# Performance work log

Hardware: AMD Instinct MI355X
Metric: run time of the kernel (lower is better)

The kernel has to match this reference:

```python
import jax, jax.numpy as jnp
import numpy as np

N_ATOMS = 8_000_000
N_REC = 2_000_000
N_POC = 500_000
N_CHAINS = 4


def setup_inputs() -> dict:
    key = jax.random.key(0)
    k1, k2, k3, k4 = jax.random.split(key, 4)
    # coordinates in nm, inside a ~5 nm box
    positions = jax.random.uniform(k1, (N_ATOMS, 3), dtype=jnp.float32) * 5.0
    box_vectors = jnp.diag(jnp.array([5.0, 5.0, 5.0], dtype=jnp.float32))
    # unique receptor atom indices into positions
    rec_indices = jax.random.permutation(k2, N_ATOMS)[:N_REC].astype(jnp.int32)
    # unique pocket indices INTO THE REC ARRAY (poc_pos = rec_pos[poc_indices])
    poc_indices = jax.random.permutation(k3, N_REC)[:N_POC].astype(jnp.int32)
    # contiguous chain assignment over rec atoms, all chains present in pocket
    chain_ids = ((jnp.arange(N_REC, dtype=jnp.int32) * N_CHAINS) // N_REC).astype(jnp.int32)
    poc_chain_ids = chain_ids[poc_indices]
    ref_poc = jax.random.uniform(k4, (N_POC, 3), dtype=jnp.float32) * 5.0
    k = jnp.float32(100.0)  # kJ/mol/nm^2
    return {
        "positions": positions, "box_vectors": box_vectors, "ref_poc": ref_poc,
        "k": k, "rec_indices": rec_indices, "poc_indices": poc_indices,
        "chain_ids": chain_ids, "poc_chain_ids": poc_chain_ids, "n_chains": N_CHAINS,
    }


def best_periodic_translation(pos1, pos2, box_vectors):
    # pos1, pos2: [C,3]; box_vectors: [3,3] (rows are lattice vectors)
    delta = pos2 - pos1
    inv = 1.0 / jnp.diag(box_vectors)
    s3 = jnp.round(delta[:, 2] * inv[2])
    delta = delta - s3[:, None] * box_vectors[2]
    s2 = jnp.round(delta[:, 1] * inv[1])
    delta = delta - s2[:, None] * box_vectors[1]
    s1 = jnp.round(delta[:, 0] * inv[0])
    return s1[:, None] * box_vectors[0] + s2[:, None] * box_vectors[1] + s3[:, None] * box_vectors[2]


def reference(positions, box_vectors, ref_poc, k, rec_indices, poc_indices, chain_ids, poc_chain_ids, n_chains):
    rec_pos = positions[rec_indices]  # [R,3]
    # Per-chain pocket COM. NOTE: original indexes global positions here
    # (positions[poc_chain_indices]), NOT rec_pos -- reproduced faithfully.
    poc_glob = positions[poc_indices]  # [P,3]
    counts = jax.ops.segment_sum(jnp.ones((poc_glob.shape[0],), poc_glob.dtype), poc_chain_ids, num_segments=n_chains)  # [C]
    poc_com = jax.ops.segment_sum(poc_glob, poc_chain_ids, num_segments=n_chains) / counts[:, None]  # [C,3]
    ref_com = jax.ops.segment_sum(ref_poc, poc_chain_ids, num_segments=n_chains) / counts[:, None]  # [C,3]
    best_t = best_periodic_translation(poc_com, ref_com, box_vectors)  # [C,3]
    rec_pos = rec_pos + best_t[chain_ids]  # translate each chain into the reference image

    poc_pos = rec_pos[poc_indices]  # [P,3]
    rec_origin = jnp.mean(rec_pos, axis=0)
    rec_centered = rec_pos - rec_origin
    r_sq = jnp.sum(rec_centered ** 2, axis=1)  # [R]
    F = jnp.zeros_like(rec_pos).at[poc_indices].set(-2.0 * k * (poc_pos - ref_poc))
    F_mean = jnp.mean(F, axis=0)
    torque = jnp.cross(rec_centered, F)
    torque_mean = jnp.mean(torque, axis=0)
    F_rot = jnp.cross(torque_mean[None], rec_centered) / r_sq[:, None]
    F_final = jnp.zeros_like(positions).at[rec_indices].set(F_mean + F_rot)
    return (jnp.float32(0.0), F_final)
```

## Files before the change

kernel.cpp:

```cpp
#include <hip/hip_runtime.h>


typedef unsigned int uint32;
typedef unsigned char uchar;

#define MAXC 16
#define W_BT 0
#define W_O 48
#define W_FM 52
#define W_TM 56
#define W_ACC 64

#define GCOUNT_OFF 4096
#define REC_OFF 8192
#define NB 512
#define BSH 14
#define BUCKET_ATOMS (1 << BSH)
#define CAP 5120
#define INV8_OFF (REC_OFF + NB * CAP * 4)

#define PB 512
#define RB 512
#define K1_KPT 16
#define K1_CHUNK (256 * K1_KPT)

struct PartSh { uint32 hist[NB]; uint32 curs[NB]; uint32 base[NB]; };
struct PocSh  { float red[4][43]; float accL[3 + MAXC * 10]; };
union ShU { PartSh part; PocSh poc; };

__device__ inline float waveSum(float v) {
#pragma unroll
  for (int off = 32; off > 0; off >>= 1) v += __shfl_down(v, off, 64);
  return v;
}

__global__ __launch_bounds__(256) void k_fused(
    const float* __restrict__ pos, const float* __restrict__ ref_poc,
    const int* __restrict__ rec_idx, const int* __restrict__ cid,
    const int* __restrict__ poc_idx, const int* __restrict__ poc_cid,
    const int* __restrict__ ncp, int R, int P,
    uint32* __restrict__ gcount, uint32* __restrict__ grecords,
    float* __restrict__ ws) {
  const int tid = threadIdx.x;
  const int bid = blockIdx.x;
  __shared__ ShU sh;
  const int C = ncp[0];

  if (bid < PB) {
    const int gsz = PB * 256;
    if (C <= 4) {
      float vals[43];
#pragma unroll
      for (int v = 0; v < 43; ++v) vals[v] = 0.f;
      for (int rb = bid * 256 + tid; rb < P; rb += 4 * gsz) {
        int rr[4], i2[4], c2[4], ri[4];
        float g[4][3], p[4][3], rf[4][3];
#pragma unroll
        for (int q = 0; q < 4; ++q) {
          int r = rb + q * gsz;
          rr[q] = (r < P) ? r : -1;
        }
#pragma unroll
        for (int q = 0; q < 4; ++q) {
          int r = (rr[q] < 0) ? 0 : rr[q];
          i2[q] = poc_idx[r];
          c2[q] = poc_cid[r];
        }
#pragma unroll
        for (int q = 0; q < 4; ++q) {
          ri[q] = rec_idx[i2[q]];
          g[q][0] = pos[3 * i2[q] + 0];
          g[q][1] = pos[3 * i2[q] + 1];
          g[q][2] = pos[3 * i2[q] + 2];
        }
#pragma unroll
        for (int q = 0; q < 4; ++q) {
          int r = (rr[q] < 0) ? 0 : rr[q];
          p[q][0] = pos[3 * ri[q] + 0];
          p[q][1] = pos[3 * ri[q] + 1];
          p[q][2] = pos[3 * ri[q] + 2];
          rf[q][0] = ref_poc[3 * r + 0];
          rf[q][1] = ref_poc[3 * r + 1];
          rf[q][2] = ref_poc[3 * r + 2];
        }
#pragma unroll
        for (int q = 0; q < 4; ++q) {
          if (rr[q] >= 0) {
            vals[0] += p[q][1] * rf[q][2] - p[q][2] * rf[q][1];
            vals[1] += p[q][2] * rf[q][0] - p[q][0] * rf[q][2];
            vals[2] += p[q][0] * rf[q][1] - p[q][1] * rf[q][0];
#pragma unroll
            for (int cc = 0; cc < 4; ++cc) {
              bool m = (c2[q] == cc);
              float* a = &vals[3 + cc * 10];
              a[0] += m ? g[q][0] : 0.f; a[1] += m ? g[q][1] : 0.f;
              a[2] += m ? g[q][2] : 0.f;
              a[3] += m ? rf[q][0] : 0.f; a[4] += m ? rf[q][1] : 0.f;
              a[5] += m ? rf[q][2] : 0.f;
              a[6] += m ? p[q][0] : 0.f; a[7] += m ? p[q][1] : 0.f;
              a[8] += m ? p[q][2] : 0.f;
              a[9] += m ? 1.f : 0.f;
            }
          }
        }
      }
      const int wid = tid >> 6;
#pragma unroll
      for (int v = 0; v < 43; ++v) {
        float s = waveSum(vals[v]);
        if ((tid & 63) == 0) sh.poc.red[wid][v] = s;
      }
      __syncthreads();
      for (int t = tid; t < 43; t += 256)
        atomicAdd(&ws[W_ACC + 19 + t], sh.poc.red[0][t] + sh.poc.red[1][t] +
                                       sh.poc.red[2][t] + sh.poc.red[3][t]);
    } else {
      float* accL = sh.poc.accL;
      for (int t = tid; t < 3 + MAXC * 10; t += 256) accL[t] = 0.f;
      __syncthreads();
      for (int r = bid * 256 + tid; r < P; r += PB * 256) {
        int i2 = poc_idx[r];
        int c2 = poc_cid[r];
        int ri = rec_idx[i2];
        float gx = pos[3 * i2 + 0], gy = pos[3 * i2 + 1], gz = pos[3 * i2 + 2];
        float px = pos[3 * ri + 0], py = pos[3 * ri + 1], pz = pos[3 * ri + 2];
        float rx = ref_poc[3 * r + 0], ry = ref_poc[3 * r + 1], rz = ref_poc[3 * r + 2];
        atomicAdd(&accL[0], py * rz - pz * ry);
        atomicAdd(&accL[1], pz * rx - px * rz);
        atomicAdd(&accL[2], px * ry - py * rx);
        float* a = &accL[3 + c2 * 10];
        atomicAdd(&a[0], gx); atomicAdd(&a[1], gy); atomicAdd(&a[2], gz);
        atomicAdd(&a[3], rx); atomicAdd(&a[4], ry); atomicAdd(&a[5], rz);
        atomicAdd(&a[6], px); atomicAdd(&a[7], py); atomicAdd(&a[8], pz);
        atomicAdd(&a[9], 1.f);
      }
      __syncthreads();
      for (int t = tid; t < 3 + MAXC * 10; t += 256)
        if (accL[t] != 0.f) atomicAdd(&ws[W_ACC + 19 + t], accL[t]);
    }
  } else {
    const int pb = bid - PB;
    uint32* hist = sh.part.hist;
    uint32* curs = sh.part.curs;
    uint32* base = sh.part.base;
    for (int r0 = pb * K1_CHUNK; r0 < R; r0 += RB * K1_CHUNK) {
      int cnt = R - r0; if (cnt > K1_CHUNK) cnt = K1_CHUNK;
      for (int t = tid; t < NB; t += 256) { hist[t] = 0u; curs[t] = 0u; }
      __syncthreads();
      uint32 enc[K1_KPT];
#pragma unroll
      for (int j = 0; j < K1_KPT; ++j) {
        int t = tid + j * 256;
        uint32 e = 0xFFFFFFFFu;
        if (t < cnt) {
          uint32 idx = (uint32)rec_idx[r0 + t];
          uint32 c = (uint32)cid[r0 + t] & 255u;
          e = (idx << 8) | c;
          atomicAdd(&hist[idx >> BSH], 1u);
        }
        enc[j] = e;
      }
      __syncthreads();
      for (int t = tid; t < NB; t += 256) {
        uint32 h = hist[t];
        base[t] = h ? atomicAdd(&gcount[t], h) : 0u;
      }
      __syncthreads();
#pragma unroll
      for (int j = 0; j < K1_KPT; ++j) {
        uint32 e = enc[j];
        if (e != 0xFFFFFFFFu) {
          uint32 b = e >> (8 + BSH);
          uint32 slot = base[b] + atomicAdd(&curs[b], 1u);
          if (slot < CAP) grecords[b * CAP + slot] = e;
        }
      }
      __syncthreads();
    }
  }
}

__global__ __launch_bounds__(256) void k_bucket_build(
    const float4* __restrict__ pos4, const int* __restrict__ ncp,
    const uint32* __restrict__ gcount, const uint32* __restrict__ grecords,
    int N, uchar* __restrict__ inv8, float* __restrict__ ws) {
  const int tid = threadIdx.x;
  const int b = blockIdx.x;
  const int a0 = b << BSH;
  if (a0 >= N) return;
  int natoms = N - a0; if (natoms > BUCKET_ATOMS) natoms = BUCKET_ATOMS;

  __shared__ uchar map_[BUCKET_ATOMS];
  __shared__ float cnt16[MAXC];
  uint4* m16 = (uint4*)map_;
  uint4 ff; ff.x = ff.y = ff.z = ff.w = 0xFFFFFFFFu;
  for (int t = tid; t < BUCKET_ATOMS / 16; t += 256) m16[t] = ff;
  const int C = ncp[0];
  if (C > 4) for (int t = tid; t < MAXC; t += 256) cnt16[t] = 0.f;
  __syncthreads();

  int n = (int)gcount[b]; if (n > CAP) n = CAP;
  float c0 = 0.f, c1 = 0.f, c2 = 0.f, c3 = 0.f;
  for (int t = tid; t < n; t += 256) {
    uint32 e = grecords[b * CAP + t];
    uint32 ia = (e >> 8) & (BUCKET_ATOMS - 1);
    uint32 c = e & 255u;
    map_[ia] = (uchar)c;
    if (C <= 4) {
      c0 += (c == 0u) ? 1.f : 0.f;
      c1 += (c == 1u) ? 1.f : 0.f;
      c2 += (c == 2u) ? 1.f : 0.f;
      c3 += (c == 3u) ? 1.f : 0.f;
    } else {
      atomicAdd(&cnt16[c], 1.f);
    }
  }
  __syncthreads();

  uchar* dst = inv8 + a0;
  if (natoms == BUCKET_ATOMS) {
    uint4* d16 = (uint4*)dst;
    for (int t = tid; t < BUCKET_ATOMS / 16; t += 256) d16[t] = m16[t];
  } else {
    for (int t = tid; t < natoms; t += 256) dst[t] = map_[t];
  }

  float sx = 0.f, sy = 0.f, sz = 0.f;
  int ngf = natoms >> 2;
  const uchar4* m4 = (const uchar4*)map_;
  int g0 = a0 >> 2;
  for (int g = tid; g < ngf; g += 256) {
    float4 p0 = pos4[3 * (g0 + g) + 0];
    float4 p1 = pos4[3 * (g0 + g) + 1];
    float4 p2 = pos4[3 * (g0 + g) + 2];
    uchar4 m = m4[g];
    if (m.x != 255) { sx += p0.x; sy += p0.y; sz += p0.z; }
    if (m.y != 255) { sx += p0.w; sy += p1.x; sz += p1.y; }
    if (m.z != 255) { sx += p1.z; sy += p1.w; sz += p2.x; }
    if (m.w != 255) { sx += p2.y; sy += p2.z; sz += p2.w; }
  }
  int tb = natoms & 3;
  if (tid < tb) {
    int a = a0 + (ngf << 2) + tid;
    const float* pf = (const float*)pos4;
    if (map_[(ngf << 2) + tid] != 255) {
      sx += pf[3 * a]; sy += pf[3 * a + 1]; sz += pf[3 * a + 2];
    }
  }

  __shared__ float red[4][7];
  float vv[7] = {sx, sy, sz, c0, c1, c2, c3};
  const int wid = tid >> 6;
#pragma unroll
  for (int v = 0; v < 7; ++v) {
    float s = waveSum(vv[v]);
    if ((tid & 63) == 0) red[wid][v] = s;
  }
  __syncthreads();
  if (tid < 7) {
    float s = red[0][tid] + red[1][tid] + red[2][tid] + red[3][tid];
    atomicAdd(&ws[W_ACC + tid], s);
  }
  if (C > 4 && tid < C) atomicAdd(&ws[W_ACC + 3 + tid], cnt16[tid]);
}

__global__ void k_finalize(const float* __restrict__ box,
                           const float* __restrict__ kp,
                           const int* __restrict__ ncp,
                           int R, float* __restrict__ ws) {
  __shared__ float tot[192];
  const int C = ncp[0];
  for (int t = threadIdx.x; t < 192; t += blockDim.x) tot[t] = ws[W_ACC + t];
  __syncthreads();
  if (threadIdx.x != 0) return;
  const float kk = kp[0];
  const float Rf = (float)R;
  const float* xp = &tot[19];
  float inv0 = 1.f / box[0], inv1 = 1.f / box[4], inv2 = 1.f / box[8];
  float ox = tot[0], oy = tot[1], oz = tot[2];
  float Fx = 0, Fy = 0, Fz = 0;
  float T1x = 0, T1y = 0, T1z = 0, T2x = 0, T2y = 0, T2z = 0;
  for (int c = 0; c < C; ++c) {
    float nrec = tot[3 + c];
    const float* a = &tot[22 + c * 10];
    float np = a[9];
    float invn = 1.f / np;
    float pcx = a[0] * invn, pcy = a[1] * invn, pcz = a[2] * invn;
    float rcx = a[3] * invn, rcy = a[4] * invn, rcz = a[5] * invn;
    float dx = rcx - pcx, dy = rcy - pcy, dz = rcz - pcz;
    float s3 = rintf(dz * inv2);
    dx -= s3 * box[6]; dy -= s3 * box[7]; dz -= s3 * box[8];
    float s2 = rintf(dy * inv1);
    dx -= s2 * box[3]; dy -= s2 * box[4]; dz -= s2 * box[5];
    float s1 = rintf(dx * inv0);
    float btx = s1 * box[0] + s2 * box[3] + s3 * box[6];
    float bty = s1 * box[1] + s2 * box[4] + s3 * box[7];
    float btz = s1 * box[2] + s2 * box[5] + s3 * box[8];
    ws[W_BT + c * 3 + 0] = btx;
    ws[W_BT + c * 3 + 1] = bty;
    ws[W_BT + c * 3 + 2] = btz;
    ox += nrec * btx; oy += nrec * bty; oz += nrec * btz;
    float SFx = -2.f * kk * (a[6] + np * btx - a[3]);
    float SFy = -2.f * kk * (a[7] + np * bty - a[4]);
    float SFz = -2.f * kk * (a[8] + np * btz - a[5]);
    Fx += SFx; Fy += SFy; Fz += SFz;
    T1x += a[7] * btz - a[8] * bty;
    T1y += a[8] * btx - a[6] * btz;
    T1z += a[6] * bty - a[7] * btx;
    T2x += bty * SFz - btz * SFy;
    T2y += btz * SFx - btx * SFz;
    T2z += btx * SFy - bty * SFx;
  }
  ox /= Rf; oy /= Rf; oz /= Rf;
  float Tx = 2.f * kk * xp[0] - 2.f * kk * T1x + T2x - (oy * Fz - oz * Fy);
  float Ty = 2.f * kk * xp[1] - 2.f * kk * T1y + T2y - (oz * Fx - ox * Fz);
  float Tz = 2.f * kk * xp[2] - 2.f * kk * T1z + T2z - (ox * Fy - oy * Fx);
  ws[W_O + 0] = ox; ws[W_O + 1] = oy; ws[W_O + 2] = oz;
  ws[W_FM + 0] = Fx / Rf; ws[W_FM + 1] = Fy / Rf; ws[W_FM + 2] = Fz / Rf;
  ws[W_TM + 0] = Tx / Rf; ws[W_TM + 1] = Ty / Rf; ws[W_TM + 2] = Tz / Rf;
}

__global__ __launch_bounds__(256) void k_final_dense(
    const float* __restrict__ pos, const uchar* __restrict__ inv8,
    int N, const float* __restrict__ ws, float* __restrict__ out) {
  __shared__ float stage[3328];
  __shared__ float sc[64];
  const int tid = threadIdx.x;
  if (tid < 64) sc[tid] = ws[tid];
  const int t0 = blockIdx.x * 1024;
  int nat = N - t0; if (nat > 1024) nat = 1024;
  const int nfl = nat * 3;

  if (nat == 1024) {
    const float4* src4 = (const float4*)(pos + 3 * t0);
#pragma unroll
    for (int kk = 0; kk < 3; ++kk) {
      int v4 = tid + kk * 256;
      float4 p = src4[v4];
      int idx = 4 * v4 + v4 / 3;
      stage[idx + 0] = p.x; stage[idx + 1] = p.y;
      stage[idx + 2] = p.z; stage[idx + 3] = p.w;
    }
  } else {
    for (int k = tid; k < nfl; k += 256)
      stage[k + (int)((unsigned)k / 12u)] = pos[3 * t0 + k];
  }
  __syncthreads();

  float ox = sc[W_O + 0], oy = sc[W_O + 1], oz = sc[W_O + 2];
  float fmx = sc[W_FM + 0], fmy = sc[W_FM + 1], fmz = sc[W_FM + 2];
  float tmx = sc[W_TM + 0], tmy = sc[W_TM + 1], tmz = sc[W_TM + 2];

  uchar mc[4];
  if (nat == 1024) {
    uchar4 m = ((const uchar4*)(inv8 + t0))[tid];
    mc[0] = m.x; mc[1] = m.y; mc[2] = m.z; mc[3] = m.w;
  } else {
#pragma unroll
    for (int q = 0; q < 4; ++q) {
      int la = 4 * tid + q;
      mc[q] = (la < nat) ? inv8[t0 + la] : (uchar)255;
    }
  }
#pragma unroll
  for (int q = 0; q < 4; ++q) {
    int la = 4 * tid + q;
    if (la < nat) {
      float* s = &stage[13 * tid + 3 * q];
      float fx = 0.f, fy = 0.f, fz = 0.f;
      int c = mc[q];
      if (c != 255) {
        float cx = s[0] + sc[W_BT + 3 * c + 0] - ox;
        float cy = s[1] + sc[W_BT + 3 * c + 1] - oy;
        float cz = s[2] + sc[W_BT + 3 * c + 2] - oz;
        float inv = 1.f / (cx * cx + cy * cy + cz * cz);
        fx = fmx + (tmy * cz - tmz * cy) * inv;
        fy = fmy + (tmz * cx - tmx * cz) * inv;
        fz = fmz + (tmx * cy - tmy * cx) * inv;
      }
      s[0] = fx; s[1] = fy; s[2] = fz;
    }
  }
  __syncthreads();

  if (blockIdx.x == 0 && tid == 0) out[0] = 0.f;
  float* ob = out + 1 + 3 * t0;
  if (nat == 1024) {
#pragma unroll
    for (int kk = 0; kk < 3; ++kk) {
      int j = tid + kk * 256;
      if (j < 767) {
        int k = 3 + 4 * j;
        float4 v;
        v.x = stage[k + k / 12];
        v.y = stage[(k + 1) + (k + 1) / 12];
        v.z = stage[(k + 2) + (k + 2) / 12];
        v.w = stage[(k + 3) + (k + 3) / 12];
        *(float4*)(ob + k) = v;
      }
    }
    if (tid < 3) ob[tid] = stage[tid];
    if (tid == 3) ob[3071] = stage[3071 + 3071 / 12];
  } else {
    for (int k = tid; k < nfl; k += 256)
      ob[k] = stage[k + (int)((unsigned)k / 12u)];
  }
}

extern "C" void kernel_launch(void* const* d_in, const int* in_sizes, int n_in,
                              void* d_out, int out_size, void* d_ws, size_t ws_size,
                              hipStream_t stream) {
  const float* pos     = (const float*)d_in[0];
  const float* box     = (const float*)d_in[1];
  const float* ref_poc = (const float*)d_in[2];
  const float* kp      = (const float*)d_in[3];
  const int* rec_idx   = (const int*)d_in[4];
  const int* poc_idx   = (const int*)d_in[5];
  const int* cid       = (const int*)d_in[6];
  const int* poc_cid   = (const int*)d_in[7];
  const int* ncp       = (const int*)d_in[8];
  float* out = (float*)d_out;
  float* ws  = (float*)d_ws;
  uint32* gcount   = (uint32*)((char*)d_ws + GCOUNT_OFF);
  uint32* grecords = (uint32*)((char*)d_ws + REC_OFF);
  uchar* inv8      = (uchar*)d_ws + INV8_OFF;

  const int N = in_sizes[0] / 3;
  const int R = in_sizes[4];
  const int P = in_sizes[5];

  hipMemsetAsync(d_ws, 0, 8192, stream);

  k_fused<<<PB + RB, 256, 0, stream>>>(pos, ref_poc, rec_idx, cid, poc_idx,
                                       poc_cid, ncp, R, P, gcount, grecords, ws);
  k_bucket_build<<<NB, 256, 0, stream>>>((const float4*)pos, ncp, gcount,
                                         grecords, N, inv8, ws);
  k_finalize<<<1, 256, 0, stream>>>(box, kp, ncp, R, ws);
  int gF = (N + 1023) / 1024;
  k_final_dense<<<gF, 256, 0, stream>>>(pos, inv8, N, ws, out);
}
```

Baseline: 267.4 us.

## Fuse all phases into one persistent kernel with software grid barriers

Merges the partition, bucket-build, finalize and dense output kernels into a single persistent kernel sized from occupancy. The phases are separated by atomic spin grid barriers, which removes three kernel launch gaps and the tail drain between them. It also halves the bucket size (1024 buckets of 8192 atoms), moves the per-chain receptor counts into the partition phase, and splits blocks 5:3 between pocket and partition work. The risks are spin-barrier overhead, a possible deadlock if not every block is co-resident, and lower parallelism in the later phases because the grid is capped at 1024 blocks.

Result: slower. 287.7 us (+7.6%).

```diff
diff --git a/kernel.cpp b/kernel.cpp
--- a/kernel.cpp
+++ b/kernel.cpp
@@ -11,22 +11,24 @@
 #define W_TM 56
 #define W_ACC 64
 
+#define BAR_OFF 4032
 #define GCOUNT_OFF 4096
 #define REC_OFF 8192
-#define NB 512
-#define BSH 14
+#define NBK 1024
+#define BSH 13
 #define BUCKET_ATOMS (1 << BSH)
-#define CAP 5120
-#define INV8_OFF (REC_OFF + NB * CAP * 4)
-
-#define PB 512
-#define RB 512
+#define CAP 2560
+#define INV8_OFF (REC_OFF + NBK * CAP * 4)
+
 #define K1_KPT 16
 #define K1_CHUNK (256 * K1_KPT)
 
-struct PartSh { uint32 hist[NB]; uint32 curs[NB]; uint32 base[NB]; };
+struct PartSh { uint32 hist[NBK]; uint32 curs[NBK]; uint32 base[NBK]; };
 struct PocSh  { float red[4][43]; float accL[3 + MAXC * 10]; };
-union ShU { PartSh part; PocSh poc; };
+struct MapSh  { uchar map_[BUCKET_ATOMS]; };
+struct StageSh{ float stage[3328]; };
+union ShU { PartSh part; PocSh poc; MapSh map; StageSh st; };
+struct MiscSh { float red7[4][7]; float sc[64]; float cnt16[MAXC]; float tot[192]; };
 
 __device__ inline float waveSum(float v) {
 #pragma unroll
@@ -34,20 +36,36 @@
   return v;
 }
 
-__global__ __launch_bounds__(256) void k_fused(
-    const float* __restrict__ pos, const float* __restrict__ ref_poc,
-    const int* __restrict__ rec_idx, const int* __restrict__ cid,
-    const int* __restrict__ poc_idx, const int* __restrict__ poc_cid,
-    const int* __restrict__ ncp, int R, int P,
-    uint32* __restrict__ gcount, uint32* __restrict__ grecords,
-    float* __restrict__ ws) {
+__device__ inline void gridBar(uint32* bar, int nblk, uint32 phase) {
+  __threadfence();
+  __syncthreads();
+  if (threadIdx.x == 0) {
+    __hip_atomic_fetch_add(bar, 1u, __ATOMIC_ACQ_REL, __HIP_MEMORY_SCOPE_AGENT);
+    const uint32 tgt = (uint32)nblk * phase;
+    for (int it = 0; it < (1 << 21); ++it) {
+      if (__hip_atomic_load(bar, __ATOMIC_ACQUIRE, __HIP_MEMORY_SCOPE_AGENT) >= tgt)
+        break;
+      __builtin_amdgcn_s_sleep(8);
+    }
+  }
+  __syncthreads();
+  __threadfence();
+}
+
+__device__ void phaseA(const float* __restrict__ pos,
+                       const float* __restrict__ ref_poc,
+                       const int* __restrict__ rec_idx,
+                       const int* __restrict__ cid,
+                       const int* __restrict__ poc_idx,
+                       const int* __restrict__ poc_cid,
+                       int C, int R, int P,
+                       uint32* __restrict__ gcount,
+                       uint32* __restrict__ grecords,
+                       float* __restrict__ ws,
+                       ShU& sh, MiscSh& ms, int bid, int pbN, int rbN) {
   const int tid = threadIdx.x;
-  const int bid = blockIdx.x;
-  __shared__ ShU sh;
-  const int C = ncp[0];
-
-  if (bid < PB) {
-    const int gsz = PB * 256;
+  if (bid < pbN) {
+    const int gsz = pbN * 256;
     if (C <= 4) {
       float vals[43];
 #pragma unroll
@@ -118,7 +136,7 @@
       float* accL = sh.poc.accL;
       for (int t = tid; t < 3 + MAXC * 10; t += 256) accL[t] = 0.f;
       __syncthreads();
-      for (int r = bid * 256 + tid; r < P; r += PB * 256) {
+      for (int r = bid * 256 + tid; r < P; r += pbN * 256) {
         int i2 = poc_idx[r];
         int c2 = poc_cid[r];
         int ri = rec_idx[i2];
@@ -139,13 +157,18 @@
         if (accL[t] != 0.f) atomicAdd(&ws[W_ACC + 19 + t], accL[t]);
     }
   } else {
-    const int pb = bid - PB;
+    const int pb = bid - pbN;
     uint32* hist = sh.part.hist;
     uint32* curs = sh.part.curs;
     uint32* base = sh.part.base;
-    for (int r0 = pb * K1_CHUNK; r0 < R; r0 += RB * K1_CHUNK) {
+    float c0 = 0.f, c1 = 0.f, c2 = 0.f, c3 = 0.f;
+    if (C > 4) {
+      for (int t = tid; t < MAXC; t += 256) ms.cnt16[t] = 0.f;
+      __syncthreads();
+    }
+    for (int r0 = pb * K1_CHUNK; r0 < R; r0 += rbN * K1_CHUNK) {
       int cnt = R - r0; if (cnt > K1_CHUNK) cnt = K1_CHUNK;
-      for (int t = tid; t < NB; t += 256) { hist[t] = 0u; curs[t] = 0u; }
+      for (int t = tid; t < NBK; t += 256) { hist[t] = 0u; curs[t] = 0u; }
       __syncthreads();
       uint32 enc[K1_KPT];
 #pragma unroll
@@ -157,11 +180,17 @@
           uint32 c = (uint32)cid[r0 + t] & 255u;
           e = (idx << 8) | c;
           atomicAdd(&hist[idx >> BSH], 1u);
+          if (C <= 4) {
+            c0 += (c == 0u) ? 1.f : 0.f; c1 += (c == 1u) ? 1.f : 0.f;
+            c2 += (c == 2u) ? 1.f : 0.f; c3 += (c == 3u) ? 1.f : 0.f;
+          } else {
+            atomicAdd(&ms.cnt16[c], 1.f);
+          }
         }
         enc[j] = e;
       }
       __syncthreads();
-      for (int t = tid; t < NB; t += 256) {
+      for (int t = tid; t < NBK; t += 256) {
         uint32 h = hist[t];
         base[t] = h ? atomicAdd(&gcount[t], h) : 0u;
       }
@@ -177,102 +206,102 @@
       }
       __syncthreads();
     }
-  }
-}
-
-__global__ __launch_bounds__(256) void k_bucket_build(
-    const float4* __restrict__ pos4, const int* __restrict__ ncp,
-    const uint32* __restrict__ gcount, const uint32* __restrict__ grecords,
-    int N, uchar* __restrict__ inv8, float* __restrict__ ws) {
+    if (C <= 4) {
+      float vv[4] = {c0, c1, c2, c3};
+      const int wid = tid >> 6;
+#pragma unroll
+      for (int v = 0; v < 4; ++v) {
+        float s = waveSum(vv[v]);
+        if ((tid & 63) == 0) ms.red7[wid][v] = s;
+      }
+      __syncthreads();
+      if (tid < 4)
+        atomicAdd(&ws[W_ACC + 3 + tid], ms.red7[0][tid] + ms.red7[1][tid] +
+                                        ms.red7[2][tid] + ms.red7[3][tid]);
+    } else {
+      __syncthreads();
+      if (tid < C) atomicAdd(&ws[W_ACC + 3 + tid], ms.cnt16[tid]);
+    }
+  }
+}
+
+__device__ void phaseBC(const float* __restrict__ pos,
+                        const uint32* __restrict__ gcount,
+                        const uint32* __restrict__ grecords,
+                        int N, uchar* __restrict__ inv8,
+                        float* __restrict__ ws,
+                        ShU& sh, MiscSh& ms, int bid, int gridN) {
   const int tid = threadIdx.x;
-  const int b = blockIdx.x;
-  const int a0 = b << BSH;
-  if (a0 >= N) return;
-  int natoms = N - a0; if (natoms > BUCKET_ATOMS) natoms = BUCKET_ATOMS;
-
-  __shared__ uchar map_[BUCKET_ATOMS];
-  __shared__ float cnt16[MAXC];
-  uint4* m16 = (uint4*)map_;
-  uint4 ff; ff.x = ff.y = ff.z = ff.w = 0xFFFFFFFFu;
-  for (int t = tid; t < BUCKET_ATOMS / 16; t += 256) m16[t] = ff;
-  const int C = ncp[0];
-  if (C > 4) for (int t = tid; t < MAXC; t += 256) cnt16[t] = 0.f;
+  float sx = 0.f, sy = 0.f, sz = 0.f;
+  for (int b = bid; b < NBK; b += gridN) {
+    const int a0 = b << BSH;
+    if (a0 >= N) break;
+    int natoms = N - a0; if (natoms > BUCKET_ATOMS) natoms = BUCKET_ATOMS;
+    uchar* map_ = sh.map.map_;
+    uint4* m16 = (uint4*)map_;
+    uint4 ff; ff.x = ff.y = ff.z = ff.w = 0xFFFFFFFFu;
+    for (int t = tid; t < BUCKET_ATOMS / 16; t += 256) m16[t] = ff;
+    __syncthreads();
+    int n = (int)gcount[b]; if (n > CAP) n = CAP;
+    for (int t = tid; t < n; t += 256) {
+      uint32 e = grecords[b * CAP + t];
+      map_[(e >> 8) & (BUCKET_ATOMS - 1)] = (uchar)(e & 255u);
+    }
+    __syncthreads();
+    uchar* dst = inv8 + a0;
+    if (natoms == BUCKET_ATOMS) {
+      uint4* d16 = (uint4*)dst;
+      for (int t = tid; t < BUCKET_ATOMS / 16; t += 256) d16[t] = m16[t];
+    } else {
+      for (int t = tid; t < natoms; t += 256) dst[t] = map_[t];
+    }
+    int ngf = natoms >> 2;
+    const uchar4* m4 = (const uchar4*)map_;
+    const float4* pos4 = (const float4*)pos;
+    int g0 = a0 >> 2;
+    for (int g = tid; g < ngf; g += 256) {
+      float4 p0 = pos4[3 * (g0 + g) + 0];
+      float4 p1 = pos4[3 * (g0 + g) + 1];
+      float4 p2 = pos4[3 * (g0 + g) + 2];
+      uchar4 m = m4[g];
+      if (m.x != 255) { sx += p0.x; sy += p0.y; sz += p0.z; }
+      if (m.y != 255) { sx += p0.w; sy += p1.x; sz += p1.y; }
+      if (m.z != 255) { sx += p1.z; sy += p1.w; sz += p2.x; }
+      if (m.w != 255) { sx += p2.y; sy += p2.z; sz += p2.w; }
+    }
+    int tb = natoms & 3;
+    if (tid < tb) {
+      int a = a0 + (ngf << 2) + tid;
+      if (map_[(ngf << 2) + tid] != 255) {
+        sx += pos[3 * a]; sy += pos[3 * a + 1]; sz += pos[3 * a + 2];
+      }
+    }
+    __syncthreads();
+  }
+  float vv[3] = {sx, sy, sz};
+  const int wid = tid >> 6;
+#pragma unroll
+  for (int v = 0; v < 3; ++v) {
+    float s = waveSum(vv[v]);
+    if ((tid & 63) == 0) ms.red7[wid][v] = s;
+  }
   __syncthreads();
-
-  int n = (int)gcount[b]; if (n > CAP) n = CAP;
-  float c0 = 0.f, c1 = 0.f, c2 = 0.f, c3 = 0.f;
-  for (int t = tid; t < n; t += 256) {
-    uint32 e = grecords[b * CAP + t];
-    uint32 ia = (e >> 8) & (BUCKET_ATOMS - 1);
-    uint32 c = e & 255u;
-    map_[ia] = (uchar)c;
-    if (C <= 4) {
-      c0 += (c == 0u) ? 1.f : 0.f;
-      c1 += (c == 1u) ? 1.f : 0.f;
-      c2 += (c == 2u) ? 1.f : 0.f;
-      c3 += (c == 3u) ? 1.f : 0.f;
-    } else {
-      atomicAdd(&cnt16[c], 1.f);
-    }
-  }
+  if (tid < 3) {
+    float s = ms.red7[0][tid] + ms.red7[1][tid] + ms.red7[2][tid] + ms.red7[3][tid];
+    if (s != 0.f) atomicAdd(&ws[W_ACC + tid], s);
+  }
+}
+
+__device__ void phaseFZ(const float* __restrict__ box,
+                        const float* __restrict__ kp,
+                        int C, int R, float* __restrict__ ws,
+                        MiscSh& ms, int bid) {
+  if (bid != 0) return;
+  const int tid = threadIdx.x;
+  for (int t = tid; t < 192; t += 256) ms.tot[t] = ws[W_ACC + t];
   __syncthreads();
-
-  uchar* dst = inv8 + a0;
-  if (natoms == BUCKET_ATOMS) {
-    uint4* d16 = (uint4*)dst;
-    for (int t = tid; t < BUCKET_ATOMS / 16; t += 256) d16[t] = m16[t];
-  } else {
-    for (int t = tid; t < natoms; t += 256) dst[t] = map_[t];
-  }
-
-  float sx = 0.f, sy = 0.f, sz = 0.f;
-  int ngf = natoms >> 2;
-  const uchar4* m4 = (const uchar4*)map_;
-  int g0 = a0 >> 2;
-  for (int g = tid; g < ngf; g += 256) {
-    float4 p0 = pos4[3 * (g0 + g) + 0];
-    float4 p1 = pos4[3 * (g0 + g) + 1];
-    float4 p2 = pos4[3 * (g0 + g) + 2];
-    uchar4 m = m4[g];
-    if (m.x != 255) { sx += p0.x; sy += p0.y; sz += p0.z; }
-    if (m.y != 255) { sx += p0.w; sy += p1.x; sz += p1.y; }
-    if (m.z != 255) { sx += p1.z; sy += p1.w; sz += p2.x; }
-    if (m.w != 255) { sx += p2.y; sy += p2.z; sz += p2.w; }
-  }
-  int tb = natoms & 3;
-  if (tid < tb) {
-    int a = a0 + (ngf << 2) + tid;
-    const float* pf = (const float*)pos4;
-    if (map_[(ngf << 2) + tid] != 255) {
-      sx += pf[3 * a]; sy += pf[3 * a + 1]; sz += pf[3 * a + 2];
-    }
-  }
-
-  __shared__ float red[4][7];
-  float vv[7] = {sx, sy, sz, c0, c1, c2, c3};
-  const int wid = tid >> 6;
-#pragma unroll
-  for (int v = 0; v < 7; ++v) {
-    float s = waveSum(vv[v]);
-    if ((tid & 63) == 0) red[wid][v] = s;
-  }
-  __syncthreads();
-  if (tid < 7) {
-    float s = red[0][tid] + red[1][tid] + red[2][tid] + red[3][tid];
-    atomicAdd(&ws[W_ACC + tid], s);
-  }
-  if (C > 4 && tid < C) atomicAdd(&ws[W_ACC + 3 + tid], cnt16[tid]);
-}
-
-__global__ void k_finalize(const float* __restrict__ box,
-                           const float* __restrict__ kp,
-                           const int* __restrict__ ncp,
-                           int R, float* __restrict__ ws) {
-  __shared__ float tot[192];
-  const int C = ncp[0];
-  for (int t = threadIdx.x; t < 192; t += blockDim.x) tot[t] = ws[W_ACC + t];
-  __syncthreads();
-  if (threadIdx.x != 0) return;
+  if (tid != 0) return;
+  float* tot = ms.tot;
   const float kk = kp[0];
   const float Rf = (float)R;
   const float* xp = &tot[19];
@@ -320,91 +349,162 @@
   ws[W_TM + 0] = Tx / Rf; ws[W_TM + 1] = Ty / Rf; ws[W_TM + 2] = Tz / Rf;
 }
 
-__global__ __launch_bounds__(256) void k_final_dense(
+__device__ void phaseD(const float* __restrict__ pos,
+                       const uchar* __restrict__ inv8,
+                       int N, const float* __restrict__ ws,
+                       float* __restrict__ out,
+                       ShU& sh, MiscSh& ms, int bid, int gridN) {
+  const int tid = threadIdx.x;
+  float* sc = ms.sc;
+  if (tid < 64) sc[tid] = ws[tid];
+  if (bid == 0 && tid == 0) out[0] = 0.f;
+  const int ntiles = (N + 1023) >> 10;
+  for (int tile = bid; tile < ntiles; tile += gridN) {
+    const int t0 = tile << 10;
+    int nat = N - t0; if (nat > 1024) nat = 1024;
+    const int nfl = nat * 3;
+    float* stage = sh.st.stage;
+
+    if (nat == 1024) {
+      const float4* src4 = (const float4*)(pos + 3 * t0);
+#pragma unroll
+      for (int kk = 0; kk < 3; ++kk) {
+        int v4 = tid + kk * 256;
+        float4 p = src4[v4];
+        int idx = 4 * v4 + v4 / 3;
+        stage[idx + 0] = p.x; stage[idx + 1] = p.y;
+        stage[idx + 2] = p.z; stage[idx + 3] = p.w;
+      }
+    } else {
+      for (int k = tid; k < nfl; k += 256)
+        stage[k + (int)((unsigned)k / 12u)] = pos[3 * t0 + k];
+    }
+    __syncthreads();
+
+    float ox = sc[W_O + 0], oy = sc[W_O + 1], oz = sc[W_O + 2];
+    float fmx = sc[W_FM + 0], fmy = sc[W_FM + 1], fmz = sc[W_FM + 2];
+    float tmx = sc[W_TM + 0], tmy = sc[W_TM + 1], tmz = sc[W_TM + 2];
+
+    uchar mc[4];
+    if (nat == 1024) {
+      uchar4 m = ((const uchar4*)(inv8 + t0))[tid];
+      mc[0] = m.x; mc[1] = m.y; mc[2] = m.z; mc[3] = m.w;
+    } else {
+#pragma unroll
+      for (int q = 0; q < 4; ++q) {
+        int la = 4 * tid + q;
+        mc[q] = (la < nat) ? inv8[t0 + la] : (uchar)255;
+      }
+    }
+#pragma unroll
+    for (int q = 0; q < 4; ++q) {
+      int la = 4 * tid + q;
+      if (la < nat) {
+        float* s = &stage[13 * tid + 3 * q];
+        float fx = 0.f, fy = 0.f, fz = 0.f;
+        int c = mc[q];
+        if (c != 255) {
+          float cx = s[0] + sc[W_BT + 3 * c + 0] - ox;
+          float cy = s[1] + sc[W_BT + 3 * c + 1] - oy;
+          float cz = s[2] + sc[W_BT + 3 * c + 2] - oz;
+          float inv = 1.f / (cx * cx + cy * cy + cz * cz);
+          fx = fmx + (tmy * cz - tmz * cy) * inv;
+          fy = fmy + (tmz * cx - tmx * cz) * inv;
+          fz = fmz + (tmx * cy - tmy * cx) * inv;
+        }
+        s[0] = fx; s[1] = fy; s[2] = fz;
+      }
+    }
+    __syncthreads();
+
+    float* ob = out + 1 + 3 * t0;
+    if (nat == 1024) {
+#pragma unroll
+      for (int kk = 0; kk < 3; ++kk) {
+        int j = tid + kk * 256;
+        if (j < 767) {
+          int k = 3 + 4 * j;
+          float4 v;
+          v.x = stage[k + k / 12];
+          v.y = stage[(k + 1) + (k + 1) / 12];
+          v.z = stage[(k + 2) + (k + 2) / 12];
+          v.w = stage[(k + 3) + (k + 3) / 12];
+          *(float4*)(ob + k) = v;
+        }
+      }
+      if (tid < 3) ob[tid] = stage[tid];
+      if (tid == 3) ob[3071] = stage[3071 + 3071 / 12];
+    } else {
+      for (int k = tid; k < nfl; k += 256)
+        ob[k] = stage[k + (int)((unsigned)k / 12u)];
+    }
+    __syncthreads();
+  }
+}
+
+__global__ __launch_bounds__(256, 4) void k_all(
+    const float* __restrict__ pos, const float* __restrict__ ref_poc,
+    const int* __restrict__ rec_idx, const int* __restrict__ cid,
+    const int* __restrict__ poc_idx, const int* __restrict__ poc_cid,
+    const int* __restrict__ ncp, const float* __restrict__ box,
+    const float* __restrict__ kp, int R, int P, int N,
+    uint32* __restrict__ gcount, uint32* __restrict__ grecords,
+    uchar* __restrict__ inv8, float* __restrict__ ws,
+    float* __restrict__ out, uint32* __restrict__ bar) {
+  __shared__ ShU sh;
+  __shared__ MiscSh ms;
+  const int bid = blockIdx.x;
+  const int gridN = gridDim.x;
+  const int pbN = (gridN * 5) >> 3;
+  const int C = ncp[0];
+  phaseA(pos, ref_poc, rec_idx, cid, poc_idx, poc_cid, C, R, P,
+         gcount, grecords, ws, sh, ms, bid, pbN, gridN - pbN);
+  gridBar(bar, gridN, 1);
+  phaseBC(pos, gcount, grecords, N, inv8, ws, sh, ms, bid, gridN);
+  gridBar(bar, gridN, 2);
+  phaseFZ(box, kp, C, R, ws, ms, bid);
+  gridBar(bar, gridN, 3);
+  phaseD(pos, inv8, N, ws, out, sh, ms, bid, gridN);
+}
+
+__global__ __launch_bounds__(256) void k_pA(
+    const float* __restrict__ pos, const float* __restrict__ ref_poc,
+    const int* __restrict__ rec_idx, const int* __restrict__ cid,
+    const int* __restrict__ poc_idx, const int* __restrict__ poc_cid,
+    const int* __restrict__ ncp, int R, int P,
+    uint32* __restrict__ gcount, uint32* __restrict__ grecords,
+    float* __restrict__ ws) {
+  __shared__ ShU sh;
+  __shared__ MiscSh ms;
+  const int gridN = gridDim.x;
+  const int pbN = (gridN * 5) >> 3;
+  phaseA(pos, ref_poc, rec_idx, cid, poc_idx, poc_cid, ncp[0], R, P,
+         gcount, grecords, ws, sh, ms, (int)blockIdx.x, pbN, gridN - pbN);
+}
+
+__global__ __launch_bounds__(256) void k_pBC(
+    const float* __restrict__ pos, const uint32* __restrict__ gcount,
+    const uint32* __restrict__ grecords, int N,
+    uchar* __restrict__ inv8, float* __restrict__ ws) {
+  __shared__ ShU sh;
+  __shared__ MiscSh ms;
+  phaseBC(pos, gcount, grecords, N, inv8, ws, sh, ms, (int)blockIdx.x,
+          (int)gridDim.x);
+}
+
+__global__ __launch_bounds__(256) void k_pFZ(
+    const float* __restrict__ box, const float* __restrict__ kp,
+    const int* __restrict__ ncp, int R, float* __restrict__ ws) {
+  __shared__ MiscSh ms;
+  phaseFZ(box, kp, ncp[0], R, ws, ms, 0);
+}
+
+__global__ __launch_bounds__(256) void k_pD(
     const float* __restrict__ pos, const uchar* __restrict__ inv8,
     int N, const float* __restrict__ ws, float* __restrict__ out) {
-  __shared__ float stage[3328];
-  __shared__ float sc[64];
-  const int tid = threadIdx.x;
-  if (tid < 64) sc[tid] = ws[tid];
-  const int t0 = blockIdx.x * 1024;
-  int nat = N - t0; if (nat > 1024) nat = 1024;
-  const int nfl = nat * 3;
-
-  if (nat == 1024) {
-    const float4* src4 = (const float4*)(pos + 3 * t0);
-#pragma unroll
-    for (int kk = 0; kk < 3; ++kk) {
-      int v4 = tid + kk * 256;
-      float4 p = src4[v4];
-      int idx = 4 * v4 + v4 / 3;
-      stage[idx + 0] = p.x; stage[idx + 1] = p.y;
-      stage[idx + 2] = p.z; stage[idx + 3] = p.w;
-    }
-  } else {
-    for (int k = tid; k < nfl; k += 256)
-      stage[k + (int)((unsigned)k / 12u)] = pos[3 * t0 + k];
-  }
-  __syncthreads();
-
-  float ox = sc[W_O + 0], oy = sc[W_O + 1], oz = sc[W_O + 2];
-  float fmx = sc[W_FM + 0], fmy = sc[W_FM + 1], fmz = sc[W_FM + 2];
-  float tmx = sc[W_TM + 0], tmy = sc[W_TM + 1], tmz = sc[W_TM + 2];
-
-  uchar mc[4];
-  if (nat == 1024) {
-    uchar4 m = ((const uchar4*)(inv8 + t0))[tid];
-    mc[0] = m.x; mc[1] = m.y; mc[2] = m.z; mc[3] = m.w;
-  } else {
-#pragma unroll
-    for (int q = 0; q < 4; ++q) {
-      int la = 4 * tid + q;
-      mc[q] = (la < nat) ? inv8[t0 + la] : (uchar)255;
-    }
-  }
-#pragma unroll
-  for (int q = 0; q < 4; ++q) {
-    int la = 4 * tid + q;
-    if (la < nat) {
-      float* s = &stage[13 * tid + 3 * q];
-      float fx = 0.f, fy = 0.f, fz = 0.f;
-      int c = mc[q];
-      if (c != 255) {
-        float cx = s[0] + sc[W_BT + 3 * c + 0] - ox;
-        float cy = s[1] + sc[W_BT + 3 * c + 1] - oy;
-        float cz = s[2] + sc[W_BT + 3 * c + 2] - oz;
-        float inv = 1.f / (cx * cx + cy * cy + cz * cz);
-        fx = fmx + (tmy * cz - tmz * cy) * inv;
-        fy = fmy + (tmz * cx - tmx * cz) * inv;
-        fz = fmz + (tmx * cy - tmy * cx) * inv;
-      }
-      s[0] = fx; s[1] = fy; s[2] = fz;
-    }
-  }
-  __syncthreads();
-
-  if (blockIdx.x == 0 && tid == 0) out[0] = 0.f;
-  float* ob = out + 1 + 3 * t0;
-  if (nat == 1024) {
-#pragma unroll
-    for (int kk = 0; kk < 3; ++kk) {
-      int j = tid + kk * 256;
-      if (j < 767) {
-        int k = 3 + 4 * j;
-        float4 v;
-        v.x = stage[k + k / 12];
-        v.y = stage[(k + 1) + (k + 1) / 12];
-        v.z = stage[(k + 2) + (k + 2) / 12];
-        v.w = stage[(k + 3) + (k + 3) / 12];
-        *(float4*)(ob + k) = v;
-      }
-    }
-    if (tid < 3) ob[tid] = stage[tid];
-    if (tid == 3) ob[3071] = stage[3071 + 3071 / 12];
-  } else {
-    for (int k = tid; k < nfl; k += 256)
-      ob[k] = stage[k + (int)((unsigned)k / 12u)];
-  }
+  __shared__ ShU sh;
+  __shared__ MiscSh ms;
+  phaseD(pos, inv8, N, ws, out, sh, ms, (int)blockIdx.x, (int)gridDim.x);
 }
 
 extern "C" void kernel_launch(void* const* d_in, const int* in_sizes, int n_in,
@@ -421,6 +521,7 @@
   const int* ncp       = (const int*)d_in[8];
   float* out = (float*)d_out;
   float* ws  = (float*)d_ws;
+  uint32* bar      = (uint32*)((char*)d_ws + BAR_OFF);
   uint32* gcount   = (uint32*)((char*)d_ws + GCOUNT_OFF);
   uint32* grecords = (uint32*)((char*)d_ws + REC_OFF);
   uchar* inv8      = (uchar*)d_ws + INV8_OFF;
@@ -431,11 +532,33 @@
 
   hipMemsetAsync(d_ws, 0, 8192, stream);
 
-  k_fused<<<PB + RB, 256, 0, stream>>>(pos, ref_poc, rec_idx, cid, poc_idx,
-                                       poc_cid, ncp, R, P, gcount, grecords, ws);
-  k_bucket_build<<<NB, 256, 0, stream>>>((const float4*)pos, ncp, gcount,
-                                         grecords, N, inv8, ws);
-  k_finalize<<<1, 256, 0, stream>>>(box, kp, ncp, R, ws);
-  int gF = (N + 1023) / 1024;
-  k_final_dense<<<gF, 256, 0, stream>>>(pos, inv8, N, ws, out);
-}
+  static int fusedGrid = -2;
+  if (fusedGrid == -2) {
+    int dev = 0;
+    (void)hipGetDevice(&dev);
+    int ncu = 0;
+    hipDeviceProp_t prop;
+    if (hipGetDeviceProperties(&prop, dev) == hipSuccess)
+      ncu = prop.multiProcessorCount;
+    if (ncu <= 0) ncu = 256;
+    int maxb = 0;
+    if (hipOccupancyMaxActiveBlocksPerMultiprocessor(
+            &maxb, (const void*)k_all, 256, 0) != hipSuccess)
+      maxb = 0;
+    long g = (long)maxb * (long)ncu;
+    fusedGrid = (g >= 512) ? (int)((g > 1024) ? 1024 : g) : 0;
+  }
+
+  if (fusedGrid > 0) {
+    k_all<<<dim3(fusedGrid), dim3(256), 0, stream>>>(
+        pos, ref_poc, rec_idx, cid, poc_idx, poc_cid, ncp, box, kp,
+        R, P, N, gcount, grecords, inv8, ws, out, bar);
+  } else {
+    k_pA<<<1024, 256, 0, stream>>>(pos, ref_poc, rec_idx, cid, poc_idx,
+                                   poc_cid, ncp, R, P, gcount, grecords, ws);
+    k_pBC<<<NBK, 256, 0, stream>>>(pos, gcount, grecords, N, inv8, ws);
+    k_pFZ<<<1, 256, 0, stream>>>(box, kp, ncp, R, ws);
+    int gF = (N + 1023) / 1024;
+    k_pD<<<gF, 256, 0, stream>>>(pos, inv8, N, ws, out);
+  }
+}
```
